# Kernel optimization log

Measured on AMD Instinct MI355X. Metric: run time of the kernel, lower is better.

The kernel has to match this reference:

```python
import jax, jax.numpy as jnp
import numpy as np

NUM_HEADS = 4
NUM_GROUPS = 8
EPS = 1e-5


def setup_inputs() -> dict:
    key = jax.random.key(0)
    ks = jax.random.split(key, 4)
    b, c, h, w = 16, 512, 32, 32
    x = jax.random.normal(ks[0], (b, c, h, w), dtype=jnp.float32)
    norm_gamma = jnp.ones((c,), dtype=jnp.float32)
    norm_beta = jnp.zeros((c,), dtype=jnp.float32)
    qkv_w = jax.random.normal(ks[1], (3 * c, c), dtype=jnp.float32) * (c ** -0.5)
    qkv_b = jnp.zeros((3 * c,), dtype=jnp.float32)
    proj_w = jax.random.normal(ks[2], (c, c), dtype=jnp.float32) * (c ** -0.5)
    proj_b = jnp.zeros((c,), dtype=jnp.float32)
    return {"x": x, "norm_gamma": norm_gamma, "norm_beta": norm_beta,
            "qkv_w": qkv_w, "qkv_b": qkv_b, "proj_w": proj_w, "proj_b": proj_b}


def reference(x, norm_gamma, norm_beta, qkv_w, qkv_b, proj_w, proj_b):
    b, c, h, w = x.shape
    nh = NUM_HEADS
    dh = c // nh
    n = h * w
    # GroupNorm(8, c): normalize over (c/G, h, w) within each group, biased var
    xg = x.reshape(b, NUM_GROUPS, -1)
    mu = jnp.mean(xg, axis=-1, keepdims=True)
    var = jnp.var(xg, axis=-1, keepdims=True)
    xn = ((xg - mu) * jax.lax.rsqrt(var + EPS)).reshape(b, c, h, w)
    xn = xn * norm_gamma[:, None, None] + norm_beta[:, None, None]
    # QKV 1x1 conv == channel matmul
    qkv = jnp.einsum('oc,bchw->bohw', qkv_w, xn) + qkv_b[:, None, None]
    q, k, v = jnp.split(qkv, 3, axis=1)  # each [b, c, h, w]

    def to_heads(t):  # [b, c, h, w] -> [b, nh, n, dh]
        return t.reshape(b, nh, dh, n).transpose(0, 1, 3, 2)

    q, k, v = to_heads(q), to_heads(k), to_heads(v)
    scale = dh ** -0.5
    attn = jax.nn.softmax(jnp.einsum('bhnd,bhmd->bhnm', q, k) * scale, axis=-1)
    out = jnp.einsum('bhnm,bhmd->bhnd', attn, v)  # [b, nh, n, dh]
    out = out.transpose(0, 1, 3, 2).reshape(b, c, h, w)
    out = jnp.einsum('oc,bchw->bohw', proj_w, out) + proj_b[:, None, None]
    return x + out
```

## Files before the change

kernel.cpp:

```cpp
#include <hip/hip_runtime.h>

typedef unsigned short u16;
typedef unsigned int   u32;

typedef __attribute__((ext_vector_type(8)))  short bf16x8;
typedef __attribute__((ext_vector_type(16))) float f32x16;
typedef __attribute__((ext_vector_type(2)))  unsigned int u32x2;
#define MFMA32(a, b, c) __builtin_amdgcn_mfma_f32_32x32x16_bf16(a, b, c, 0, 0, 0)

__device__ __forceinline__ float bf2f(u16 h) { return __uint_as_float(((u32)h) << 16); }
__device__ __forceinline__ u16 f2bf(float f) {
  u32 u = __float_as_uint(f);
  u += 0x7fffu + ((u >> 16) & 1u);
  return (u16)(u >> 16);
}
__device__ __forceinline__ void unpack8(uint4 u, float* f) {
  f[0] = __uint_as_float(u.x << 16); f[1] = __uint_as_float(u.x & 0xffff0000u);
  f[2] = __uint_as_float(u.y << 16); f[3] = __uint_as_float(u.y & 0xffff0000u);
  f[4] = __uint_as_float(u.z << 16); f[5] = __uint_as_float(u.z & 0xffff0000u);
  f[6] = __uint_as_float(u.w << 16); f[7] = __uint_as_float(u.w & 0xffff0000u);
}
__device__ __forceinline__ void unpack4(uint2 u, float* f) {
  f[0] = __uint_as_float(u.x << 16); f[1] = __uint_as_float(u.x & 0xffff0000u);
  f[2] = __uint_as_float(u.y << 16); f[3] = __uint_as_float(u.y & 0xffff0000u);
}

template <bool F>
__device__ __forceinline__ void load8(const void* p, size_t idx, float* f) {
  if constexpr (F) {
    const float4* q = (const float4*)((const float*)p + idx);
    float4 a = q[0], b = q[1];
    f[0] = a.x; f[1] = a.y; f[2] = a.z; f[3] = a.w;
    f[4] = b.x; f[5] = b.y; f[6] = b.z; f[7] = b.w;
  } else {
    unpack8(*(const uint4*)((const u16*)p + idx), f);
  }
}
template <bool F>
__device__ __forceinline__ void load4(const void* p, size_t idx, float* f) {
  if constexpr (F) {
    float4 a = *(const float4*)((const float*)p + idx);
    f[0] = a.x; f[1] = a.y; f[2] = a.z; f[3] = a.w;
  } else {
    unpack4(*(const uint2*)((const u16*)p + idx), f);
  }
}
template <bool F>
__device__ __forceinline__ float load1(const void* p, size_t idx) {
  if constexpr (F) return ((const float*)p)[idx];
  else return bf2f(((const u16*)p)[idx]);
}

__device__ __forceinline__ void gl2lds16(const void* g, void* l) {
  __builtin_amdgcn_global_load_lds(
      (const __attribute__((address_space(1))) void*)g,
      (__attribute__((address_space(3))) void*)l, 16, 0, 0);
}

__global__ void detect_dtype(const void* __restrict__ x, int* __restrict__ flag) {
  if (threadIdx.x == 0 && blockIdx.x == 0) {
    const u32* p = (const u32*)x;
    int sane = 0;
    for (int i = 0; i < 256; ++i) {
      u32 e = (p[i] >> 7) & 0xFFu;
      sane += (e >= 100u && e <= 150u) ? 1 : 0;
    }
    *flag = (sane < 192) ? 1 : 0;
  }
}

__global__ void signal_ws(u16* __restrict__ out, int n) {
  int i = blockIdx.x * 256 + threadIdx.x;
  if (i < n) out[i] = 0x42C8;
}

#define SM_SCALE 0.08838834764831843f
#define QSC 0.12751743f


__global__ void __launch_bounds__(256) wconv_rt(const void* __restrict__ qkvw,
                                                const void* __restrict__ qkvb,
                                                u16* __restrict__ dst,
                                                const int* __restrict__ flag) {
  const bool F = (flag[0] != 0);
  int i = (blockIdx.x * 256 + threadIdx.x) * 8;
  if (i >= 787968) return;
  if (!F) {
    uint4 v = (i < 786432) ? *(const uint4*)((const u16*)qkvw + i)
                           : *(const uint4*)((const u16*)qkvb + (i - 786432));
    *(uint4*)(dst + i) = v;
  } else {
    const float* src = (i < 786432) ? ((const float*)qkvw + i)
                                    : ((const float*)qkvb + (i - 786432));
    float f[8];
    float4 a = *(const float4*)src, b = *(const float4*)(src + 4);
    f[0]=a.x; f[1]=a.y; f[2]=a.z; f[3]=a.w; f[4]=b.x; f[5]=b.y; f[6]=b.z; f[7]=b.w;
    u32 w0 = (u32)f2bf(f[0]) | ((u32)f2bf(f[1]) << 16);
    u32 w1 = (u32)f2bf(f[2]) | ((u32)f2bf(f[3]) << 16);
    u32 w2 = (u32)f2bf(f[4]) | ((u32)f2bf(f[5]) << 16);
    u32 w3 = (u32)f2bf(f[6]) | ((u32)f2bf(f[7]) << 16);
    *(uint4*)(dst + i) = make_uint4(w0, w1, w2, w3);
  }
}

template <bool F>
__device__ __forceinline__ void gn_norm_body(
    const void* __restrict__ x, const void* __restrict__ gamma,
    const void* __restrict__ beta, u16* __restrict__ xT,
    int g, int b, int tid,
    float* ssum, float* ssq, float* scb, float* bsb, float (*Tf)[65]) {
  const size_t base = (size_t)(b * 512 + g * 64) * 1024;
  float sum = 0.f, sq = 0.f;
  for (int i = tid; i < 8192; i += 256) {
    float f[8]; load8<F>(x, base + (size_t)i * 8, f);
#pragma unroll
    for (int m = 0; m < 8; ++m) { sum += f[m]; sq += f[m] * f[m]; }
  }
  ssum[tid] = sum; ssq[tid] = sq; __syncthreads();
  for (int off = 128; off > 0; off >>= 1) {
    if (tid < off) { ssum[tid] += ssum[tid + off]; ssq[tid] += ssq[tid + off]; }
    __syncthreads();
  }
  if (tid < 64) {
    float mu  = ssum[0] * (1.f / 65536.f);
    float var = ssq[0] * (1.f / 65536.f) - mu * mu;
    float s = load1<F>(gamma, g * 64 + tid) * rsqrtf(var + 1e-5f);
    scb[tid] = s;
    bsb[tid] = load1<F>(beta, g * 64 + tid) - mu * s;
  }
  __syncthreads();

  for (int s0 = 0; s0 < 1024; s0 += 64) {
#pragma unroll
    for (int half = 0; half < 2; ++half) {
      int idx = tid + half * 256;
      int c_loc = idx >> 3, s8 = (idx & 7) * 8;
      float f[8];
      load8<F>(x, base + (size_t)c_loc * 1024 + s0 + s8, f);
      float sm = scb[c_loc], ba = bsb[c_loc];
#pragma unroll
      for (int m = 0; m < 8; ++m) Tf[s8 + m][c_loc] = f[m] * sm + ba;
    }
    __syncthreads();
#pragma unroll
    for (int half = 0; half < 2; ++half) {
      int idx = tid + half * 256;
      int s_loc = idx >> 3, c8 = (idx & 7) * 8;
      u32 pk[4];
#pragma unroll
      for (int m = 0; m < 4; ++m)
        pk[m] = (u32)f2bf(Tf[s_loc][c8 + 2 * m]) |
                ((u32)f2bf(Tf[s_loc][c8 + 2 * m + 1]) << 16);
      *(uint4*)(xT + (size_t)(b * 1024 + s0 + s_loc) * 512 + g * 64 + c8) =
          make_uint4(pk[0], pk[1], pk[2], pk[3]);
    }
    __syncthreads();
  }
}

__global__ void __launch_bounds__(256) gn_norm_rt(const void* __restrict__ x,
                                                  const void* __restrict__ gamma,
                                                  const void* __restrict__ beta,
                                                  u16* __restrict__ xT,
                                                  const int* __restrict__ flag) {
  __shared__ float ssum[256], ssq[256], scb[64], bsb[64];
  __shared__ float Tf[64][65];
  const int g = blockIdx.x, b = blockIdx.y, tid = threadIdx.x;
  if (flag[0] != 0) gn_norm_body<true >(x, gamma, beta, xT, g, b, tid, ssum, ssq, scb, bsb, Tf);
  else              gn_norm_body<false>(x, gamma, beta, xT, g, b, tid, ssum, ssq, scb, bsb, Tf);
}

__global__ void __launch_bounds__(256, 4)
gemm_qkv(const u16* __restrict__ xT, const u16* __restrict__ wbf,
         u16* __restrict__ qkT, u16* __restrict__ Vbuf) {
  const bool vrole = (blockIdx.y >= 8);
  const int n0 = blockIdx.x * 128;
  const int m0 = (vrole ? (int)blockIdx.y - 8 : (int)blockIdx.y) * 128;
  const int b  = blockIdx.z;
  __shared__ __align__(16) u16 At[8192];
  __shared__ __align__(16) u16 Bt[8192];
  const int tid = threadIdx.x;
  const int w = tid >> 6, lane = tid & 63;
  const int lo = lane & 31, hi = lane >> 5;
  const int wm = w >> 1, wn = w & 1;
  const u16* bias = wbf + 786432;
  const u16* Ab = vrole ? (wbf + 524288) : (xT + (size_t)b * 524288);
  const u16* Bb = vrole ? (xT + (size_t)b * 524288) : wbf;
  u16* outp = vrole ? (Vbuf + (size_t)b * 524288) : (qkT + (size_t)b * 1048576);
  const int srow = lane >> 3, spc = lane & 7;

  f32x16 cA[2][2];
#pragma unroll
  for (int i = 0; i < 2; ++i)
#pragma unroll
    for (int j = 0; j < 2; ++j)
#pragma unroll
      for (int r = 0; r < 16; ++r) cA[i][j][r] = 0.f;

  for (int kt = 0; kt < 8; ++kt) {
    const int kb = kt * 64;
#pragma unroll
    for (int c = 0; c < 4; ++c) {
      int grp = w * 4 + c;
      int row = grp * 8 + srow;
      int lc  = spc ^ (row & 7);
      gl2lds16(Ab + (size_t)(m0 + row) * 512 + kb + lc * 8, &At[grp * 512]);
      gl2lds16(Bb + (size_t)(n0 + row) * 512 + kb + lc * 8, &Bt[grp * 512]);
    }
    __syncthreads();
#pragma unroll
    for (int k16 = 0; k16 < 4; ++k16) {
      const int lc = k16 * 2 + hi;
      const int rA0 = wm * 64 + lo,  rA1 = rA0 + 32;
      const int rB0 = wn * 64 + lo,  rB1 = rB0 + 32;
      bf16x8 a0 = *(const bf16x8*)&At[rA0 * 64 + ((lc ^ (rA0 & 7)) << 3)];
      bf16x8 a1 = *(const bf16x8*)&At[rA1 * 64 + ((lc ^ (rA1 & 7)) << 3)];
      bf16x8 b0 = *(const bf16x8*)&Bt[rB0 * 64 + ((lc ^ (rB0 & 7)) << 3)];
      bf16x8 b1 = *(const bf16x8*)&Bt[rB1 * 64 + ((lc ^ (rB1 & 7)) << 3)];
      cA[0][0] = MFMA32(a0, b0, cA[0][0]);
      cA[0][1] = MFMA32(a0, b1, cA[0][1]);
      cA[1][0] = MFMA32(a1, b0, cA[1][0]);
      cA[1][1] = MFMA32(a1, b1, cA[1][1]);
    }
    __syncthreads();
  }

  float bcol[2] = {0.f, 0.f};
  if (!vrole) {
    bcol[0] = bf2f(bias[n0 + wn * 64 + lo]);
    bcol[1] = bf2f(bias[n0 + wn * 64 + 32 + lo]);
  }
#pragma unroll
  for (int mt = 0; mt < 2; ++mt)
#pragma unroll
    for (int nt = 0; nt < 2; ++nt) {
      const int nbase = n0 + wn * 64 + nt * 32;
#pragma unroll
      for (int r = 0; r < 16; ++r) {
        int m = m0 + wm * 64 + mt * 32 + (r & 3) + 8 * (r >> 2) + 4 * hi;
        int n = nbase + lo;
        float v = cA[mt][nt][r];
        if (!vrole) {
          v += bcol[nt];
          if (nbase < 512) v *= QSC;
        } else {
          v += bf2f(bias[1024 + m]);
        }
        outp[(size_t)m * 1024 + n] = f2bf(v);
      }
    }
}

template <bool F>
__device__ __forceinline__ void proj_body(const void* __restrict__ A,
                                          const u16* __restrict__ B,
                                          const void* __restrict__ bias,
                                          const void* __restrict__ resid,
                                          void* __restrict__ outp,
                                          int n0, int m0, int b, int tid,
                                          u16 (*At)[72], u16 (*Bt)[72]) {
  const int w = tid >> 6, lane = tid & 63;
  const int lo = lane & 31, hi = lane >> 5;
  const int wm = w >> 1, wn = w & 1;
  const size_t bBase = (size_t)b * 524288;

  f32x16 cA[2][2];
#pragma unroll
  for (int i = 0; i < 2; ++i)
#pragma unroll
    for (int j = 0; j < 2; ++j)
#pragma unroll
      for (int r = 0; r < 16; ++r) cA[i][j][r] = 0.f;

  for (int kt = 0; kt < 8; ++kt) {
#pragma unroll
    for (int i = 0; i < 4; ++i) {
      int idx = tid + i * 256;
      int row = idx >> 3, kc = (idx & 7) * 8;
      int k = kt * 64 + kc;
      {
        if constexpr (F) {
          float f[8]; load8<true>(A, (size_t)(m0 + row) * 512 + k, f);
          u32 w0 = (u32)f2bf(f[0]) | ((u32)f2bf(f[1]) << 16);
          u32 w1 = (u32)f2bf(f[2]) | ((u32)f2bf(f[3]) << 16);
          u32 w2 = (u32)f2bf(f[4]) | ((u32)f2bf(f[5]) << 16);
          u32 w3 = (u32)f2bf(f[6]) | ((u32)f2bf(f[7]) << 16);
          *(uint4*)&At[row][kc] = make_uint4(w0, w1, w2, w3);
        } else {
          *(uint4*)&At[row][kc] =
              *(const uint4*)((const u16*)A + (size_t)(m0 + row) * 512 + k);
        }
      }
      *(uint4*)&Bt[row][kc] =
          *(const uint4*)(B + bBase + (size_t)(n0 + row) * 512 + k);
    }
    __syncthreads();
#pragma unroll
    for (int k16 = 0; k16 < 4; ++k16) {
      const int ko = k16 * 16 + hi * 8;
      bf16x8 a0 = *(const bf16x8*)&At[wm * 64 + lo][ko];
      bf16x8 a1 = *(const bf16x8*)&At[wm * 64 + 32 + lo][ko];
      bf16x8 b0 = *(const bf16x8*)&Bt[wn * 64 + lo][ko];
      bf16x8 b1 = *(const bf16x8*)&Bt[wn * 64 + 32 + lo][ko];
      cA[0][0] = MFMA32(a0, b0, cA[0][0]);
      cA[0][1] = MFMA32(a0, b1, cA[0][1]);
      cA[1][0] = MFMA32(a1, b0, cA[1][0]);
      cA[1][1] = MFMA32(a1, b1, cA[1][1]);
    }
    __syncthreads();
  }

#pragma unroll
  for (int mt = 0; mt < 2; ++mt)
#pragma unroll
    for (int nt = 0; nt < 2; ++nt) {
#pragma unroll
      for (int r = 0; r < 16; ++r) {
        int m = m0 + wm * 64 + mt * 32 + (r & 3) + 8 * (r >> 2) + 4 * hi;
        int n = n0 + wn * 64 + nt * 32 + lo;
        float v = cA[mt][nt][r];
        v += load1<F>(bias, m);
        v += load1<F>(resid, bBase + (size_t)m * 1024 + n);
        size_t off = bBase + (size_t)m * 1024 + n;
        if constexpr (F) ((float*)outp)[off] = v;
        else             ((u16*)outp)[off] = f2bf(v);
      }
    }
}

__global__ void __launch_bounds__(256, 4)
proj_rt(const void* __restrict__ projw, const u16* __restrict__ aout,
        const void* __restrict__ projb, const void* __restrict__ x,
        void* __restrict__ outp, const int* __restrict__ flag) {
  __shared__ __align__(16) u16 At[128][72];
  __shared__ __align__(16) u16 Bt[128][72];
  const int n0 = blockIdx.x * 128, m0 = blockIdx.y * 128, b = blockIdx.z;
  if (flag[0] != 0) proj_body<true >(projw, aout, projb, x, outp, n0, m0, b, threadIdx.x, At, Bt);
  else              proj_body<false>(projw, aout, projb, x, outp, n0, m0, b, threadIdx.x, At, Bt);
}

__global__ void __launch_bounds__(256, 2) attn4(const u16* __restrict__ qkT,
                                                const u16* __restrict__ V,
                                                u16* __restrict__ aout) {
  const int bh = blockIdx.x;
  const int q0 = blockIdx.y * 128;
  const int b = bh >> 2, h = bh & 3;
  const u16* qt = qkT + (size_t)b * 1048576;
  const u16* vb = V + (size_t)b * 524288 + (size_t)(h * 128) * 1024;
  __shared__ __align__(16) u16 smem[32768];
  const int tid = threadIdx.x;
  const int w = tid >> 6, lane = tid & 63;
  const int lo = lane & 31, hi = lane >> 5;

#pragma unroll
  for (int c = 0; c < 8; ++c) {
    int grp = w * 8 + c;
    int row = grp * 4 + (lane >> 4);
    int lc  = (lane & 15) ^ (row & 7);
    gl2lds16(qt + (size_t)(q0 + row) * 1024 + h * 128 + lc * 8, &smem[grp * 512]);
  }
#pragma unroll
  for (int c = 0; c < 4; ++c) {
    int grp = w * 4 + c;
    { int row = grp * 4 + (lane >> 4);
      int lc  = (lane & 15) ^ (row & 7);
      gl2lds16(qt + (size_t)row * 1024 + 512 + h * 128 + lc * 8,
               &smem[16384 + grp * 512]); }
    { int row = grp * 8 + (lane >> 3);
      int lc  = (lane & 7) ^ (row & 7);
      gl2lds16(vb + (size_t)row * 1024 + lc * 8,
               &smem[16384 + 8192 + grp * 512]); }
  }
  __syncthreads();
  bf16x8 qf[8];
  {
    const int row = 32 * w + lo;
#pragma unroll
    for (int k16 = 0; k16 < 8; ++k16) {
      int lc = k16 * 2 + hi;
      qf[k16] = *(const bf16x8*)&smem[row * 128 + ((lc ^ (row & 7)) << 3)];
    }
  }
  __syncthreads();

  f32x16 o[4];
  float lp = 0.f;
#pragma unroll
  for (int dt = 0; dt < 4; ++dt)
#pragma unroll
    for (int r = 0; r < 16; ++r) o[dt][r] = 0.f;

  for (int kt = 0; kt < 16; ++kt) {
    const u16* rb = &smem[((kt & 1) ^ 1) << 14];
    u16* wbuf = &smem[(kt & 1) << 14];

    if (kt < 15) {
      const int k0n = (kt + 1) * 64;
#pragma unroll
      for (int c = 0; c < 4; ++c) {
        int grp = w * 4 + c;
        { int row = grp * 4 + (lane >> 4);
          int lc  = (lane & 15) ^ (row & 7);
          gl2lds16(qt + (size_t)(k0n + row) * 1024 + 512 + h * 128 + lc * 8,
                   wbuf + grp * 512); }
        { int row = grp * 8 + (lane >> 3);
          int lc  = (lane & 7) ^ (row & 7);
          gl2lds16(vb + (size_t)row * 1024 + k0n + lc * 8,
                   wbuf + 8192 + grp * 512); }
      }
    }

    f32x16 s0, s1;
#pragma unroll
    for (int r = 0; r < 16; ++r) { s0[r] = 0.f; s1[r] = 0.f; }
    __builtin_amdgcn_s_setprio(1);
#pragma unroll
    for (int k16 = 0; k16 < 8; ++k16) {
      const int lc = k16 * 2 + hi;
      const int r0 = lo, r1 = lo + 32;
      bf16x8 kf0 = *(const bf16x8*)&rb[r0 * 128 + ((lc ^ (r0 & 7)) << 3)];
      bf16x8 kf1 = *(const bf16x8*)&rb[r1 * 128 + ((lc ^ (r1 & 7)) << 3)];
      s0 = MFMA32(kf0, qf[k16], s0);
      s1 = MFMA32(kf1, qf[k16], s1);
    }
    __builtin_amdgcn_s_setprio(0);

#pragma unroll
    for (int r = 0; r < 16; ++r) {
      s0[r] = exp2f(s0[r]);
      s1[r] = exp2f(s1[r]);
      lp += s0[r] + s1[r];
    }

    bf16x8 pa[4];
#define MKPA(ps, rb0, dst) do {                                               \
      u32 qa0, qa1, qb0, qb1;                                                 \
      asm("v_cvt_pk_bf16_f32 %0, %1, %2" : "=v"(qa0)                          \
          : "v"((ps)[(rb0) + 0]), "v"((ps)[(rb0) + 1]));                      \
      asm("v_cvt_pk_bf16_f32 %0, %1, %2" : "=v"(qa1)                          \
          : "v"((ps)[(rb0) + 2]), "v"((ps)[(rb0) + 3]));                      \
      asm("v_cvt_pk_bf16_f32 %0, %1, %2" : "=v"(qb0)                          \
          : "v"((ps)[(rb0) + 4]), "v"((ps)[(rb0) + 5]));                      \
      asm("v_cvt_pk_bf16_f32 %0, %1, %2" : "=v"(qb1)                          \
          : "v"((ps)[(rb0) + 6]), "v"((ps)[(rb0) + 7]));                      \
      u32x2 r0 = __builtin_amdgcn_permlane32_swap(qa0, qb0, false, false);    \
      u32x2 r1 = __builtin_amdgcn_permlane32_swap(qa1, qb1, false, false);    \
      union { u32 u[4]; bf16x8 v8; } pk_;                                     \
      pk_.u[0] = r0[0]; pk_.u[1] = r1[0]; pk_.u[2] = r0[1]; pk_.u[3] = r1[1]; \
      dst = pk_.v8;                                                           \
    } while (0)
    MKPA(s0, 0, pa[0]);
    MKPA(s0, 8, pa[1]);
    MKPA(s1, 0, pa[2]);
    MKPA(s1, 8, pa[3]);
#undef MKPA

    __builtin_amdgcn_s_setprio(1);
#pragma unroll
    for (int t = 0; t < 4; ++t) {
      const int lc = t * 2 + hi;
#pragma unroll
      for (int dt = 0; dt < 4; ++dt) {
        const int row = dt * 32 + lo;
        bf16x8 bv = *(const bf16x8*)&rb[8192 + row * 64 + ((lc ^ (row & 7)) << 3)];
        o[dt] = MFMA32(pa[t], bv, o[dt]);
      }
    }
    __builtin_amdgcn_s_setprio(0);
    __syncthreads();
  }

  float linv = 1.f / (lp + __shfl_xor(lp, 32));
#pragma unroll
  for (int r = 0; r < 16; ++r) {
    int pat = (r & 3) + 8 * (r >> 2) + 4 * hi;
    float lr = __shfl(linv, pat);
    int q = q0 + 32 * w + pat;
    size_t base = (size_t)(b * 1024 + q) * 512 + h * 128;
    aout[base +  0 + lo] = f2bf(o[0][r] * lr);
    aout[base + 32 + lo] = f2bf(o[1][r] * lr);
    aout[base + 64 + lo] = f2bf(o[2][r] * lr);
    aout[base + 96 + lo] = f2bf(o[3][r] * lr);
  }
}


template <bool F>
__global__ void __launch_bounds__(256) gn_stats(const void* __restrict__ x,
                                                const void* __restrict__ gamma,
                                                const void* __restrict__ beta,
                                                float* __restrict__ sc,
                                                float* __restrict__ bs,
                                                const int* __restrict__ flag) {
  if ((flag[0] != 0) != F) return;
  const int g = blockIdx.x, b = blockIdx.y;
  const int tid = threadIdx.x;
  const size_t base = (size_t)(b * 512 + g * 64) * 1024;
  float sum = 0.f, sq = 0.f;
  for (int i = tid; i < 8192; i += 256) {
    float f[8]; load8<F>(x, base + (size_t)i * 8, f);
#pragma unroll
    for (int m = 0; m < 8; ++m) { sum += f[m]; sq += f[m] * f[m]; }
  }
  __shared__ float ssum[256], ssq[256];
  ssum[tid] = sum; ssq[tid] = sq; __syncthreads();
  for (int off = 128; off > 0; off >>= 1) {
    if (tid < off) { ssum[tid] += ssum[tid + off]; ssq[tid] += ssq[tid + off]; }
    __syncthreads();
  }
  if (tid < 64) {
    float mu  = ssum[0] * (1.f / 65536.f);
    float var = ssq[0] * (1.f / 65536.f) - mu * mu;
    int c = g * 64 + tid;
    float s = load1<F>(gamma, c) * rsqrtf(var + 1e-5f);
    sc[b * 512 + c] = s;
    bs[b * 512 + c] = load1<F>(beta, c) - mu * s;
  }
}

template <bool F, bool BEXT, bool FOUT>
__global__ void __launch_bounds__(256) gemm64(const void* __restrict__ A,
                                              const void* __restrict__ B,
                                              const float* __restrict__ sc,
                                              const float* __restrict__ bs,
                                              const void* __restrict__ bias,
                                              const void* __restrict__ resid,
                                              void* __restrict__ outp,
                                              int mrows, int donorm, int bstride,
                                              const int* __restrict__ flag) {
  if ((flag[0] != 0) != F) return;
  const int s0 = blockIdx.x * 64;
  const int o0 = blockIdx.y * 64;
  const int b  = blockIdx.z;
  __shared__ __align__(16) float At[64][36];
  __shared__ __align__(16) float Bt[64][36];
  const int tid = threadIdx.x;
  const int ty = tid >> 4, tx = tid & 15;
  const int i0 = ty * 4, j0 = tx * 4;
  const int arow = tid >> 2, akc = (tid & 3) * 8;
  const int brow = tid >> 3, bnc = (tid & 7) * 8;
  float acc[4][4] = {};

  for (int kt = 0; kt < 512; kt += 32) {
    float af[8];
    load8<F>(A, (size_t)(o0 + arow) * 512 + akc + kt, af);
    *(float4*)&At[arow][akc]     = make_float4(af[0], af[1], af[2], af[3]);
    *(float4*)&At[arow][akc + 4] = make_float4(af[4], af[5], af[6], af[7]);
    const int c = kt + brow;
    float bf[8];
    load8<(BEXT && F)>(B, (size_t)(b * bstride + c) * 1024 + s0 + bnc, bf);
    float smul = 1.f, badd = 0.f;
    if (donorm) { smul = sc[b * 512 + c]; badd = bs[b * 512 + c]; }
#pragma unroll
    for (int m = 0; m < 8; ++m) Bt[bnc + m][brow] = bf[m] * smul + badd;
    __syncthreads();
#pragma unroll
    for (int kq = 0; kq < 8; ++kq) {
      float4 a0 = *(const float4*)&At[i0 + 0][kq * 4];
      float4 a1 = *(const float4*)&At[i0 + 1][kq * 4];
      float4 a2 = *(const float4*)&At[i0 + 2][kq * 4];
      float4 a3 = *(const float4*)&At[i0 + 3][kq * 4];
      float4 c0 = *(const float4*)&Bt[j0 + 0][kq * 4];
      float4 c1 = *(const float4*)&Bt[j0 + 1][kq * 4];
      float4 c2 = *(const float4*)&Bt[j0 + 2][kq * 4];
      float4 c3 = *(const float4*)&Bt[j0 + 3][kq * 4];
#define DOT4(ii, jj, AV, CV) acc[ii][jj] += AV.x * CV.x + AV.y * CV.y + AV.z * CV.z + AV.w * CV.w;
      DOT4(0,0,a0,c0) DOT4(0,1,a0,c1) DOT4(0,2,a0,c2) DOT4(0,3,a0,c3)
      DOT4(1,0,a1,c0) DOT4(1,1,a1,c1) DOT4(1,2,a1,c2) DOT4(1,3,a1,c3)
      DOT4(2,0,a2,c0) DOT4(2,1,a2,c1) DOT4(2,2,a2,c2) DOT4(2,3,a2,c3)
      DOT4(3,0,a3,c0) DOT4(3,1,a3,c1) DOT4(3,2,a3,c2) DOT4(3,3,a3,c3)
#undef DOT4
    }
    __syncthreads();
  }
#pragma unroll
  for (int ii = 0; ii < 4; ++ii) {
    const int o = o0 + i0 + ii;
    const float bb = load1<F>(bias, o);
    float v[4];
#pragma unroll
    for (int jj = 0; jj < 4; ++jj) v[jj] = acc[ii][jj] + bb;
    if (resid) {
      float xf[4];
      load4<F>(resid, (size_t)(b * 512 + o) * 1024 + s0 + j0, xf);
#pragma unroll
      for (int jj = 0; jj < 4; ++jj) v[jj] += xf[jj];
    }
    const size_t ooff = (size_t)(b * mrows + o) * 1024 + s0 + j0;
    if constexpr (FOUT) {
      *(float4*)((float*)outp + ooff) = make_float4(v[0], v[1], v[2], v[3]);
    } else {
      uint2 pk;
      pk.x = (u32)f2bf(v[0]) | ((u32)f2bf(v[1]) << 16);
      pk.y = (u32)f2bf(v[2]) | ((u32)f2bf(v[3]) << 16);
      *(uint2*)((u16*)outp + ooff) = pk;
    }
  }
}

__global__ void __launch_bounds__(256, 2) attn_old(u16* __restrict__ qkv) {
  const int q0 = blockIdx.x * 128;
  const int bh = blockIdx.y;
  const int b = bh >> 2, h = bh & 3;
  u16* qp = qkv + (size_t)(b * 1536 + h * 128) * 1024;
  const u16* kp = qp + (size_t)512 * 1024;
  const u16* vp = qp + (size_t)1024 * 1024;
  __shared__ __align__(16) u16 Qt[128][136];
  __shared__ __align__(16) u16 Kt[32][136];
  __shared__ __align__(16) u16 Vt[128][40];
  __shared__ __align__(16) u16 Pt[128][40];
  const int tid = threadIdx.x;
  const int w = tid >> 6, lane = tid & 63;
  const int lo = lane & 31, hi = lane >> 5;

  for (int idx = tid; idx < 2048; idx += 256) {
    int d = idx >> 4, s8 = (idx & 15) * 8;
    uint4 qv = *(const uint4*)(qp + (size_t)d * 1024 + q0 + s8);
    const u16* qs = (const u16*)&qv;
#pragma unroll
    for (int m = 0; m < 8; ++m) Qt[s8 + m][d] = qs[m];
  }
  __syncthreads();
  bf16x8 qf[8];
#pragma unroll
  for (int kq = 0; kq < 8; ++kq)
    qf[kq] = *(const bf16x8*)&Qt[32 * w + lo][kq * 16 + hi * 8];

  f32x16 o0, o1, o2, o3;
  float lp[16];
#pragma unroll
  for (int r = 0; r < 16; ++r) { o0[r] = 0.f; o1[r] = 0.f; o2[r] = 0.f; o3[r] = 0.f; lp[r] = 0.f; }

  for (int kt = 0; kt < 32; ++kt) {
    const int k0 = kt * 32;
    __syncthreads();
    for (int idx = tid; idx < 512; idx += 256) {
      int d = idx >> 2, s8 = (idx & 3) * 8;
      uint4 kv = *(const uint4*)(kp + (size_t)d * 1024 + k0 + s8);
      const u16* ks = (const u16*)&kv;
#pragma unroll
      for (int m = 0; m < 8; ++m) Kt[s8 + m][d] = ks[m];
      *(uint4*)&Vt[d][s8] = *(const uint4*)(vp + (size_t)d * 1024 + k0 + s8);
    }
    __syncthreads();
    f32x16 acc;
#pragma unroll
    for (int r = 0; r < 16; ++r) acc[r] = 0.f;
#pragma unroll
    for (int kq = 0; kq < 8; ++kq) {
      bf16x8 bq = *(const bf16x8*)&Kt[lo][kq * 16 + hi * 8];
      acc = MFMA32(qf[kq], bq, acc);
    }
#pragma unroll
    for (int r = 0; r < 16; ++r) {
      float pe = __expf(acc[r] * SM_SCALE);
      lp[r] += pe;
      int row = (r & 3) + 8 * (r >> 2) + 4 * hi;
      Pt[32 * w + row][lo] = f2bf(pe);
    }
    __syncthreads();
#pragma unroll
    for (int kq2 = 0; kq2 < 2; ++kq2) {
      bf16x8 a2 = *(const bf16x8*)&Pt[32 * w + lo][kq2 * 16 + hi * 8];
      bf16x8 b0 = *(const bf16x8*)&Vt[ 0 + lo][kq2 * 16 + hi * 8];
      bf16x8 b1 = *(const bf16x8*)&Vt[32 + lo][kq2 * 16 + hi * 8];
      bf16x8 b2 = *(const bf16x8*)&Vt[64 + lo][kq2 * 16 + hi * 8];
      bf16x8 b3 = *(const bf16x8*)&Vt[96 + lo][kq2 * 16 + hi * 8];
      o0 = MFMA32(a2, b0, o0);
      o1 = MFMA32(a2, b1, o1);
      o2 = MFMA32(a2, b2, o2);
      o3 = MFMA32(a2, b3, o3);
    }
  }
#pragma unroll
  for (int r = 0; r < 16; ++r) {
    float su = lp[r];
    su += __shfl_xor(su, 1);  su += __shfl_xor(su, 2);
    su += __shfl_xor(su, 4);  su += __shfl_xor(su, 8);
    su += __shfl_xor(su, 16);
    float linv = 1.f / su;
    int row = (r & 3) + 8 * (r >> 2) + 4 * hi;
    int q = q0 + 32 * w + row;
    size_t base = (size_t)(b * 1536 + h * 128) * 1024 + q;
    qkv[base + (size_t)( 0 + lo) * 1024] = f2bf(o0[r] * linv);
    qkv[base + (size_t)(32 + lo) * 1024] = f2bf(o1[r] * linv);
    qkv[base + (size_t)(64 + lo) * 1024] = f2bf(o2[r] * linv);
    qkv[base + (size_t)(96 + lo) * 1024] = f2bf(o3[r] * linv);
  }
}

extern "C" void kernel_launch(void* const* d_in, const int* in_sizes, int n_in,
                              void* d_out, int out_size, void* d_ws, size_t ws_size,
                              hipStream_t stream) {
  const void* x     = d_in[0];
  const void* gamma = d_in[1];
  const void* beta  = d_in[2];
  const void* qkvw  = d_in[3];
  const void* qkvb  = d_in[4];
  const void* projw = d_in[5];
  const void* projb = d_in[6];

  char* ws = (char*)d_ws;
  const size_t MB = 1024 * 1024;
  const size_t FAST_NEED = 64 * MB + 64;
  const size_t OLD_NEED  = 48 * MB + 256 + 2 * 16 * 512 * 4;

  if (ws_size >= FAST_NEED) {
    u16* xT   = (u16*)ws;
    u16* qkT  = (u16*)(ws + 16 * MB);
    u16* Vbuf = (u16*)(ws + 48 * MB);
    int* flag = (int*)(ws + 64 * MB);
    u16* wbf  = (u16*)d_out;

    detect_dtype<<<1, 64, 0, stream>>>(x, flag);
    wconv_rt<<<385, 256, 0, stream>>>(qkvw, qkvb, wbf, flag);
    gn_norm_rt<<<dim3(8, 16), 256, 0, stream>>>(x, gamma, beta, xT, flag);

    gemm_qkv<<<dim3(8, 12, 16), 256, 0, stream>>>(xT, wbf, qkT, Vbuf);

    attn4<<<dim3(64, 8), 256, 0, stream>>>(qkT, Vbuf, xT);

    proj_rt<<<dim3(8, 4, 16), 256, 0, stream>>>(projw, xT, projb, x, d_out, flag);
    return;
  }

  if (ws_size < OLD_NEED) {
    signal_ws<<<(out_size + 255) / 256, 256, 0, stream>>>((u16*)d_out, out_size);
    return;
  }

  const size_t QKV_BYTES = (size_t)16 * 1536 * 1024 * 2;
  u16* qkv  = (u16*)ws;
  int* flag = (int*)(ws + QKV_BYTES);
  float* sc = (float*)(ws + QKV_BYTES + 256);
  float* bs = sc + 16 * 512;

  detect_dtype<<<1, 64, 0, stream>>>(x, flag);
  gn_stats<false><<<dim3(8, 16), 256, 0, stream>>>(x, gamma, beta, sc, bs, flag);
  gn_stats<true ><<<dim3(8, 16), 256, 0, stream>>>(x, gamma, beta, sc, bs, flag);
  gemm64<false, true, false><<<dim3(16, 24, 16), 256, 0, stream>>>(
      qkvw, x, sc, bs, qkvb, nullptr, qkv, 1536, 1, 512, flag);
  gemm64<true, true, false><<<dim3(16, 24, 16), 256, 0, stream>>>(
      qkvw, x, sc, bs, qkvb, nullptr, qkv, 1536, 1, 512, flag);
  attn_old<<<dim3(8, 64), 256, 0, stream>>>(qkv);
  gemm64<false, false, false><<<dim3(16, 8, 16), 256, 0, stream>>>(
      projw, qkv, sc, bs, projb, x, d_out, 512, 0, 1536, flag);
  gemm64<true, false, true><<<dim3(16, 8, 16), 256, 0, stream>>>(
      projw, qkv, sc, bs, projb, x, d_out, 512, 0, 1536, flag);
}
```

Before: 254.0 us.

## Double-buffer GroupNorm transpose and QKV GEMM tiles, remap blocks, drop setprio

The GroupNorm transpose tile is double-buffered so one barrier per 64-column chunk can be removed. The QKV GEMM double-buffers its LDS A/B tiles and prefetches the next k-slice while computing the current one. It also remaps the linear block index to change scheduling locality, and relaxes launch bounds to 2 blocks per CU to make room for the doubled LDS. The attention kernel drops its s_setprio hints around the MFMA sections. In exchange, LDS use doubles and occupancy may fall.

```diff
diff --git a/kernel.cpp b/kernel.cpp
--- a/kernel.cpp
+++ b/kernel.cpp
@@ -108,7 +108,7 @@
     const void* __restrict__ x, const void* __restrict__ gamma,
     const void* __restrict__ beta, u16* __restrict__ xT,
     int g, int b, int tid,
-    float* ssum, float* ssq, float* scb, float* bsb, float (*Tf)[65]) {
+    float* ssum, float* ssq, float* scb, float* bsb, float (*Tf)[64][65]) {
   const size_t base = (size_t)(b * 512 + g * 64) * 1024;
   float sum = 0.f, sq = 0.f;
   for (int i = tid; i < 8192; i += 256) {
@@ -131,6 +131,7 @@
   __syncthreads();
 
   for (int s0 = 0; s0 < 1024; s0 += 64) {
+    const int pb = (s0 >> 6) & 1;
 #pragma unroll
     for (int half = 0; half < 2; ++half) {
       int idx = tid + half * 256;
@@ -139,7 +140,7 @@
       load8<F>(x, base + (size_t)c_loc * 1024 + s0 + s8, f);
       float sm = scb[c_loc], ba = bsb[c_loc];
 #pragma unroll
-      for (int m = 0; m < 8; ++m) Tf[s8 + m][c_loc] = f[m] * sm + ba;
+      for (int m = 0; m < 8; ++m) Tf[pb][s8 + m][c_loc] = f[m] * sm + ba;
     }
     __syncthreads();
 #pragma unroll
@@ -149,12 +150,11 @@
       u32 pk[4];
 #pragma unroll
       for (int m = 0; m < 4; ++m)
-        pk[m] = (u32)f2bf(Tf[s_loc][c8 + 2 * m]) |
-                ((u32)f2bf(Tf[s_loc][c8 + 2 * m + 1]) << 16);
+        pk[m] = (u32)f2bf(Tf[pb][s_loc][c8 + 2 * m]) |
+                ((u32)f2bf(Tf[pb][s_loc][c8 + 2 * m + 1]) << 16);
       *(uint4*)(xT + (size_t)(b * 1024 + s0 + s_loc) * 512 + g * 64 + c8) =
           make_uint4(pk[0], pk[1], pk[2], pk[3]);
     }
-    __syncthreads();
   }
 }
 
@@ -164,21 +164,27 @@
                                                   u16* __restrict__ xT,
                                                   const int* __restrict__ flag) {
   __shared__ float ssum[256], ssq[256], scb[64], bsb[64];
-  __shared__ float Tf[64][65];
+  __shared__ float Tf[2][64][65];
   const int g = blockIdx.x, b = blockIdx.y, tid = threadIdx.x;
   if (flag[0] != 0) gn_norm_body<true >(x, gamma, beta, xT, g, b, tid, ssum, ssq, scb, bsb, Tf);
   else              gn_norm_body<false>(x, gamma, beta, xT, g, b, tid, ssum, ssq, scb, bsb, Tf);
 }
 
-__global__ void __launch_bounds__(256, 4)
+__global__ void __launch_bounds__(256, 2)
 gemm_qkv(const u16* __restrict__ xT, const u16* __restrict__ wbf,
          u16* __restrict__ qkT, u16* __restrict__ Vbuf) {
-  const bool vrole = (blockIdx.y >= 8);
-  const int n0 = blockIdx.x * 128;
-  const int m0 = (vrole ? (int)blockIdx.y - 8 : (int)blockIdx.y) * 128;
-  const int b  = blockIdx.z;
-  __shared__ __align__(16) u16 At[8192];
-  __shared__ __align__(16) u16 Bt[8192];
+  const int linear  = (int)blockIdx.x + 8 * ((int)blockIdx.y + 12 * (int)blockIdx.z);
+  const int logical = (linear & 7) * 192 + (linear >> 3);
+  const int lx   = logical & 7;
+  const int rest = logical >> 3;
+  const int ly   = rest % 12;
+  const int lz   = rest / 12;
+  const bool vrole = (ly >= 8);
+  const int n0 = lx * 128;
+  const int m0 = (vrole ? ly - 8 : ly) * 128;
+  const int b  = lz;
+  __shared__ __align__(16) u16 At[2][8192];
+  __shared__ __align__(16) u16 Bt[2][8192];
   const int tid = threadIdx.x;
   const int w = tid >> 6, lane = tid & 63;
   const int lo = lane & 31, hi = lane >> 5;
@@ -197,26 +203,35 @@
 #pragma unroll
       for (int r = 0; r < 16; ++r) cA[i][j][r] = 0.f;
 
+#define QKV_STAGE(KB, AD, BD) do {                                            \
+    _Pragma("unroll")                                                         \
+    for (int c = 0; c < 4; ++c) {                                             \
+      int grp = w * 4 + c;                                                    \
+      int row = grp * 8 + srow;                                               \
+      int lc  = spc ^ (row & 7);                                              \
+      gl2lds16(Ab + (size_t)(m0 + row) * 512 + (KB) + lc * 8, &(AD)[grp * 512]); \
+      gl2lds16(Bb + (size_t)(n0 + row) * 512 + (KB) + lc * 8, &(BD)[grp * 512]); \
+    }                                                                         \
+  } while (0)
+
+  QKV_STAGE(0, At[0], Bt[0]);
+  __syncthreads();
+
   for (int kt = 0; kt < 8; ++kt) {
-    const int kb = kt * 64;
-#pragma unroll
-    for (int c = 0; c < 4; ++c) {
-      int grp = w * 4 + c;
-      int row = grp * 8 + srow;
-      int lc  = spc ^ (row & 7);
-      gl2lds16(Ab + (size_t)(m0 + row) * 512 + kb + lc * 8, &At[grp * 512]);
-      gl2lds16(Bb + (size_t)(n0 + row) * 512 + kb + lc * 8, &Bt[grp * 512]);
-    }
-    __syncthreads();
+    const u16* at = At[kt & 1];
+    const u16* bt = Bt[kt & 1];
+    if (kt < 7) {
+      QKV_STAGE((kt + 1) * 64, At[(kt & 1) ^ 1], Bt[(kt & 1) ^ 1]);
+    }
 #pragma unroll
     for (int k16 = 0; k16 < 4; ++k16) {
       const int lc = k16 * 2 + hi;
       const int rA0 = wm * 64 + lo,  rA1 = rA0 + 32;
       const int rB0 = wn * 64 + lo,  rB1 = rB0 + 32;
-      bf16x8 a0 = *(const bf16x8*)&At[rA0 * 64 + ((lc ^ (rA0 & 7)) << 3)];
-      bf16x8 a1 = *(const bf16x8*)&At[rA1 * 64 + ((lc ^ (rA1 & 7)) << 3)];
-      bf16x8 b0 = *(const bf16x8*)&Bt[rB0 * 64 + ((lc ^ (rB0 & 7)) << 3)];
-      bf16x8 b1 = *(const bf16x8*)&Bt[rB1 * 64 + ((lc ^ (rB1 & 7)) << 3)];
+      bf16x8 a0 = *(const bf16x8*)&at[rA0 * 64 + ((lc ^ (rA0 & 7)) << 3)];
+      bf16x8 a1 = *(const bf16x8*)&at[rA1 * 64 + ((lc ^ (rA1 & 7)) << 3)];
+      bf16x8 b0 = *(const bf16x8*)&bt[rB0 * 64 + ((lc ^ (rB0 & 7)) << 3)];
+      bf16x8 b1 = *(const bf16x8*)&bt[rB1 * 64 + ((lc ^ (rB1 & 7)) << 3)];
       cA[0][0] = MFMA32(a0, b0, cA[0][0]);
       cA[0][1] = MFMA32(a0, b1, cA[0][1]);
       cA[1][0] = MFMA32(a1, b0, cA[1][0]);
@@ -224,6 +239,7 @@
     }
     __syncthreads();
   }
+#undef QKV_STAGE
 
   float bcol[2] = {0.f, 0.f};
   if (!vrole) {
@@ -413,7 +429,6 @@
     f32x16 s0, s1;
 #pragma unroll
     for (int r = 0; r < 16; ++r) { s0[r] = 0.f; s1[r] = 0.f; }
-    __builtin_amdgcn_s_setprio(1);
 #pragma unroll
     for (int k16 = 0; k16 < 8; ++k16) {
       const int lc = k16 * 2 + hi;
@@ -423,7 +438,6 @@
       s0 = MFMA32(kf0, qf[k16], s0);
       s1 = MFMA32(kf1, qf[k16], s1);
     }
-    __builtin_amdgcn_s_setprio(0);
 
 #pragma unroll
     for (int r = 0; r < 16; ++r) {
@@ -455,7 +469,6 @@
     MKPA(s1, 8, pa[3]);
 #undef MKPA
 
-    __builtin_amdgcn_s_setprio(1);
 #pragma unroll
     for (int t = 0; t < 4; ++t) {
       const int lc = t * 2 + hi;
@@ -466,7 +479,6 @@
         o[dt] = MFMA32(pa[t], bv, o[dt]);
       }
     }
-    __builtin_amdgcn_s_setprio(0);
     __syncthreads();
   }
 
```

Result: slower. 265.9 us (+4.7%).
